# Performance work log

Hardware: AMD Instinct MI355X
Metric: run time of the kernel (lower is better)

## Reference

```python
import jax, jax.numpy as jnp
import numpy as np
import math

B, S, D, H, L, V, MAXLEN = 4, 2047, 256, 8, 2, 32000, 2048
DK = D // H
DFF = 2 * D
EPS = 1e-5


def make_pe(max_len, d):
    pos = jnp.arange(max_len, dtype=jnp.float32)[:, None]
    div = jnp.exp(jnp.arange(0, d, 2, dtype=jnp.float32) * (-math.log(10000.0) / d))
    pe = jnp.zeros((max_len, d), dtype=jnp.float32)
    pe = pe.at[:, 0::2].set(jnp.sin(pos * div))
    pe = pe.at[:, 1::2].set(jnp.cos(pos * div))
    return pe[None]  # [1, max_len, d]


def setup_inputs() -> dict:
    key = jax.random.key(0)
    ks = jax.random.split(key, 16)
    s = 0.02
    T = S + 1
    return {
        "embeddings": jax.random.normal(ks[0], (B, D), jnp.float32),
        "output_tokens": jax.random.randint(ks[1], (B, S), 0, V, jnp.int64),
        "causal_mask": jnp.tril(jnp.ones((T, T), jnp.int32))[None, None],  # [1,1,T,T]
        "key_padding_mask": jnp.ones((B, 1, 1, T), jnp.int32),
        "tok_emb": jax.random.normal(ks[2], (V, D), jnp.float32) * s,
        "pe": make_pe(MAXLEN, D),
        "Wq": jax.random.normal(ks[3], (L, D, D), jnp.float32) * s,
        "Wk": jax.random.normal(ks[4], (L, D, D), jnp.float32) * s,
        "Wv": jax.random.normal(ks[5], (L, D, D), jnp.float32) * s,
        "Wo": jax.random.normal(ks[6], (L, D, D), jnp.float32) * s,
        "bo": jnp.zeros((L, D), jnp.float32),
        "ln1_g": jnp.ones((L, D), jnp.float32),
        "ln1_b": jnp.zeros((L, D), jnp.float32),
        "W1": jax.random.normal(ks[7], (L, D, DFF), jnp.float32) * s,
        "b1": jnp.zeros((L, DFF), jnp.float32),
        "W2": jax.random.normal(ks[8], (L, DFF, D), jnp.float32) * s,
        "b2": jnp.zeros((L, D), jnp.float32),
        "ln2_g": jnp.ones((L, D), jnp.float32),
        "ln2_b": jnp.zeros((L, D), jnp.float32),
    }


def layer_norm(x, g, b):
    mu = jnp.mean(x, axis=-1, keepdims=True)
    var = jnp.mean(jnp.square(x - mu), axis=-1, keepdims=True)
    return (x - mu) * jax.lax.rsqrt(var + EPS) * g + b


def attention(x, Wq, Wk, Wv, Wo, bo, causal_mask, key_padding_mask):
    b, t, d = x.shape
    q = (x @ Wq).reshape(b, t, H, DK)
    k = (x @ Wk).reshape(b, t, H, DK)
    v = (x @ Wv).reshape(b, t, H, DK)
    scores = jnp.einsum('bqhd,bkhd->bhqk', q, k) / math.sqrt(DK)  # [B,H,T,T]
    neg = jnp.float32(-jnp.inf)
    scores = jnp.where(causal_mask == 0, neg, scores)
    scores = jnp.where(key_padding_mask == 0, neg, scores)
    attn = jax.nn.softmax(scores, axis=-1)
    out = jnp.einsum('bhqk,bkhd->bqhd', attn, v).reshape(b, t, d)
    return out @ Wo + bo


def reference(embeddings, output_tokens, causal_mask, key_padding_mask,
              tok_emb, pe, Wq, Wk, Wv, Wo, bo, ln1_g, ln1_b,
              W1, b1, W2, b2, ln2_g, ln2_b):
    emb_tok = tok_emb[output_tokens]                       # [B,S,D]
    x = jnp.concatenate([embeddings[:, None, :], emb_tok], axis=1)  # [B,T,D]
    x = x + pe[:, :x.shape[1]]
    for l in range(L):
        a = attention(x, Wq[l], Wk[l], Wv[l], Wo[l], bo[l], causal_mask, key_padding_mask)
        x = layer_norm(x + a, ln1_g[l], ln1_b[l])
        ff = jax.nn.relu(x @ W1[l] + b1[l]) @ W2[l] + b2[l]
        x = layer_norm(x + ff, ln2_g[l], ln2_b[l])
    return x[:, 1:, :]  # drop the prepended embedding position
```

## Files before the change

kernel.cpp:

```cpp
#include <hip/hip_runtime.h>
#include <cstdint>
#include <cstddef>

#define B_   4
#define S_   2047
#define T_   2048
#define D_   256
#define H_   8
#define DK_  32
#define DFF_ 512
#define L_   2

typedef short          s8v  __attribute__((ext_vector_type(8)));
typedef float          f4v  __attribute__((ext_vector_type(4)));
typedef unsigned short u4v  __attribute__((ext_vector_type(4)));
typedef unsigned short u8v  __attribute__((ext_vector_type(8)));
typedef unsigned int   u2v  __attribute__((ext_vector_type(2)));
typedef unsigned int   uint32;

union U8 { u8v v; unsigned short e[8]; };

__device__ __forceinline__ float bf2f(unsigned short h) {
    unsigned int u = ((unsigned int)h) << 16;
    float f; __builtin_memcpy(&f, &u, 4); return f;
}
__device__ __forceinline__ unsigned short f2bf(float f) {
    unsigned int u; __builtin_memcpy(&u, &f, 4);
    u += 0x7fffu + ((u >> 16) & 1u);
    return (unsigned short)(u >> 16);
}
__device__ __forceinline__ uint32 pack_bf2(float lo, float hi) {
    uint32 a, b;
    __builtin_memcpy(&a, &lo, 4); __builtin_memcpy(&b, &hi, 4);
    a += 0x8000u; b += 0x8000u;
    return __builtin_amdgcn_perm(b, a, 0x07060302);
}

#define QSCALE2 0.25503485951542068f

__global__ __launch_bounds__(256) void prep_k(
    const float* __restrict__ emb, const int* __restrict__ toks,
    const float* __restrict__ tokE, const float* __restrict__ pe,
    unsigned short* __restrict__ X,
    const float* __restrict__ Wq, const float* __restrict__ Wk,
    const float* __restrict__ Wv, const float* __restrict__ Wo,
    const float* __restrict__ W1, const float* __restrict__ W2,
    unsigned short* __restrict__ WqkvT, unsigned short* __restrict__ WoT,
    unsigned short* __restrict__ W1T, unsigned short* __restrict__ W2T)
{
    __shared__ float tile[32][33];
    if (blockIdx.x < 1024) {
        int idx = blockIdx.x * 256 + threadIdx.x;
        int d8 = (idx & 31) * 8;
        int t  = (idx >> 5) & (T_ - 1);
        int b  = idx >> 16;
        const float* src = (t == 0) ? (emb + b * D_)
                                    : (tokE + (size_t)toks[b * S_ + t - 1] * D_);
        const float* p = pe + (size_t)t * D_ + d8;
        U8 o;
#pragma unroll
        for (int j = 0; j < 8; ++j) o.e[j] = f2bf(src[d8 + j] + p[j]);
        *(u8v*)(X + (size_t)(b * T_ + t) * D_ + d8) = o.v;
        return;
    }
    int idx = blockIdx.x - 1024;
    const float* src; unsigned short* dst; int R, C, tr, tc;
    if (idx < 512) {
        int w = idx >> 7, rem = idx & 127, l = rem >> 6, t = rem & 63;
        tr = t >> 3; tc = t & 7; R = 256; C = 256;
        src = (w == 0 ? Wq : w == 1 ? Wk : w == 2 ? Wv : Wo) + (size_t)l * 65536;
        dst = (w < 3) ? WqkvT + (size_t)l * 196608 + (size_t)w * 65536
                      : WoT + (size_t)l * 65536;
    } else if (idx < 768) {
        int rem = idx - 512, l = rem >> 7, t = rem & 127;
        tr = t >> 4; tc = t & 15; R = 256; C = 512;
        src = W1 + (size_t)l * 131072; dst = W1T + (size_t)l * 131072;
    } else {
        int rem = idx - 768, l = rem >> 7, t = rem & 127;
        tr = t >> 3; tc = t & 7; R = 512; C = 256;
        src = W2 + (size_t)l * 131072; dst = W2T + (size_t)l * 131072;
    }
    int x = threadIdx.x & 31, y = threadIdx.x >> 5;
    int r0 = tr * 32, c0 = tc * 32;
#pragma unroll
    for (int i = 0; i < 32; i += 8) tile[y + i][x] = src[(size_t)(r0 + y + i) * C + c0 + x];
    __syncthreads();
#pragma unroll
    for (int i = 0; i < 32; i += 8)
        dst[(size_t)(c0 + y + i) * R + r0 + x] = f2bf(tile[x][y + i]);
}

__global__ __launch_bounds__(256) void gemm64_k(
    const unsigned short* __restrict__ A, const unsigned short* __restrict__ WT,
    const float* __restrict__ bias,
    unsigned short* __restrict__ oq, unsigned short* __restrict__ ok,
    unsigned short* __restrict__ ov, unsigned short* __restrict__ out,
    int K, int Ntot, int mode)
{
    __shared__ unsigned short At[64 * 72];
    __shared__ unsigned short Wt[64 * 72];
    const int tid = threadIdx.x;
    const int wave = tid >> 6, lane = tid & 63, l15 = lane & 15, quad = lane >> 4;
    const int m0 = blockIdx.x * 64, n0g = blockIdx.y * 64;

    f4v acc[4];
#pragma unroll
    for (int i = 0; i < 4; ++i) acc[i] = (f4v){0.f, 0.f, 0.f, 0.f};

    const int arow = tid >> 2, acg = (tid & 3) * 16;
    const unsigned short* ag = A + (size_t)(m0 + arow) * K + acg;
    const unsigned short* wg = WT + (size_t)(n0g + arow) * K + acg;
    u8v a0 = *(const u8v*)ag, a1 = *(const u8v*)(ag + 8);
    u8v w0 = *(const u8v*)wg, w1 = *(const u8v*)(wg + 8);

    const int niter = K >> 6;
    for (int kk = 0; kk < niter; ++kk) {
        *(u8v*)&At[arow * 72 + acg] = a0; *(u8v*)&At[arow * 72 + acg + 8] = a1;
        *(u8v*)&Wt[arow * 72 + acg] = w0; *(u8v*)&Wt[arow * 72 + acg + 8] = w1;
        __syncthreads();
        if (kk + 1 < niter) {
            int o = (kk + 1) * 64;
            a0 = *(const u8v*)(ag + o); a1 = *(const u8v*)(ag + o + 8);
            w0 = *(const u8v*)(wg + o); w1 = *(const u8v*)(wg + o + 8);
        }
#pragma unroll
        for (int ks = 0; ks < 2; ++ks) {
            s8v aF = *(const s8v*)&At[(wave * 16 + l15) * 72 + ks * 32 + quad * 8];
#pragma unroll
            for (int nt = 0; nt < 4; ++nt) {
                s8v wF = *(const s8v*)&Wt[(nt * 16 + l15) * 72 + ks * 32 + quad * 8];
                acc[nt] = __builtin_amdgcn_mfma_f32_16x16x32_bf16(aF, wF, acc[nt], 0, 0, 0);
            }
        }
        __syncthreads();
    }

    const int b = m0 >> 11, t0 = m0 & (T_ - 1);
    if (mode == 0) {
        int sub = blockIdx.y >> 2;
        int cb  = (blockIdx.y & 3) * 64;
        if (sub < 2) {
            unsigned short* dst = sub ? ok : oq;
            float sc = sub ? 1.f : QSCALE2;
#pragma unroll
            for (int nt = 0; nt < 4; ++nt) {
                int c = cb + nt * 16 + l15, hh = c >> 5, dk = c & 31;
#pragma unroll
                for (int r = 0; r < 4; ++r) {
                    int t = t0 + wave * 16 + quad * 4 + r;
                    dst[((size_t)(b * H_ + hh) * T_ + t) * DK_ + dk] = f2bf(acc[nt][r] * sc);
                }
            }
        } else {
            unsigned short* Vb = At;
#pragma unroll
            for (int nt = 0; nt < 4; ++nt) {
                int base = (nt * 16 + l15) * 72 + wave * 16 + quad * 4;
                *(uint32*)&Vb[base]     = pack_bf2(acc[nt][0], acc[nt][1]);
                *(uint32*)&Vb[base + 2] = pack_bf2(acc[nt][2], acc[nt][3]);
            }
            __syncthreads();
            int c = tid >> 2, chunk = tid & 3;
            int cg = cb + c, hh = cg >> 5, dk = cg & 31;
            unsigned short* dst = ov + ((size_t)(b * H_ + hh) * DK_ + dk) * T_ + t0 + chunk * 16;
            u8v v0 = *(u8v*)&Vb[c * 72 + chunk * 16];
            u8v v1 = *(u8v*)&Vb[c * 72 + chunk * 16 + 8];
            *(u8v*)dst = v0; *(u8v*)(dst + 8) = v1;
        }
    } else {
#pragma unroll
        for (int nt = 0; nt < 4; ++nt) {
            int c = n0g + nt * 16 + l15;
            float bv = bias[c];
#pragma unroll
            for (int r = 0; r < 4; ++r) {
                float v = acc[nt][r] + bv;
                v = v > 0.f ? v : 0.f;
                out[(size_t)(m0 + wave * 16 + quad * 4 + r) * Ntot + c] = f2bf(v);
            }
        }
    }
}

__global__ __launch_bounds__(256) void gemm16_k(
    const unsigned short* __restrict__ A, const unsigned short* __restrict__ WT,
    const float* __restrict__ bias, const unsigned short* __restrict__ resid,
    const float* __restrict__ gamma, const float* __restrict__ beta,
    unsigned short* __restrict__ out, int K)
{
    __shared__ unsigned short At[16 * 72];
    __shared__ unsigned short Wt[256 * 72];
    const int tid = threadIdx.x;
    const int wave = tid >> 6, lane = tid & 63, l15 = lane & 15, quad = lane >> 4;
    const int m0 = blockIdx.x * 16;

    f4v acc[4];
#pragma unroll
    for (int i = 0; i < 4; ++i) acc[i] = (f4v){0.f, 0.f, 0.f, 0.f};

    const int arow = tid >> 4, ac4 = (tid & 15) * 4;
    const unsigned short* ag = A + (size_t)(m0 + arow) * K + ac4;
    const unsigned short* wg = WT + (size_t)tid * K;
    u4v aR = *(const u4v*)ag;
    u8v wR[8];
#pragma unroll
    for (int j = 0; j < 8; ++j) wR[j] = *(const u8v*)(wg + j * 8);

    const int niter = K >> 6;
    for (int kk = 0; kk < niter; ++kk) {
        *(u4v*)&At[arow * 72 + ac4] = aR;
#pragma unroll
        for (int j = 0; j < 8; ++j) *(u8v*)&Wt[tid * 72 + j * 8] = wR[j];
        __syncthreads();
        if (kk + 1 < niter) {
            int o = (kk + 1) * 64;
            aR = *(const u4v*)(ag + o);
#pragma unroll
            for (int j = 0; j < 8; ++j) wR[j] = *(const u8v*)(wg + o + j * 8);
        }
#pragma unroll
        for (int ks = 0; ks < 2; ++ks) {
            s8v aF = *(const s8v*)&At[l15 * 72 + ks * 32 + quad * 8];
#pragma unroll
            for (int nt = 0; nt < 4; ++nt) {
                s8v wF = *(const s8v*)&Wt[(wave * 64 + nt * 16 + l15) * 72 + ks * 32 + quad * 8];
                acc[nt] = __builtin_amdgcn_mfma_f32_16x16x32_bf16(aF, wF, acc[nt], 0, 0, 0);
            }
        }
        __syncthreads();
    }

    const int rbase = quad * 4;
    float* LNs = (float*)Wt;
    float* LNq = LNs + 64;
    float ps[4] = {0, 0, 0, 0}, pq[4] = {0, 0, 0, 0};
#pragma unroll
    for (int nt = 0; nt < 4; ++nt) {
        int c = wave * 64 + nt * 16 + l15;
        float bv = bias[c];
#pragma unroll
        for (int r = 0; r < 4; ++r) {
            float v = acc[nt][r] + bv + bf2f(resid[(size_t)(m0 + rbase + r) * D_ + c]);
            acc[nt][r] = v;
            ps[r] += v; pq[r] += v * v;
        }
    }
#pragma unroll
    for (int r = 0; r < 4; ++r) {
        float s = ps[r], q = pq[r];
        s += __shfl_xor(s, 1); q += __shfl_xor(q, 1);
        s += __shfl_xor(s, 2); q += __shfl_xor(q, 2);
        s += __shfl_xor(s, 4); q += __shfl_xor(q, 4);
        s += __shfl_xor(s, 8); q += __shfl_xor(q, 8);
        if (l15 == 0) { LNs[(rbase + r) * 4 + wave] = s; LNq[(rbase + r) * 4 + wave] = q; }
    }
    __syncthreads();
    float mu[4], rsig[4];
#pragma unroll
    for (int r = 0; r < 4; ++r) {
        int row = rbase + r;
        float s = LNs[row * 4] + LNs[row * 4 + 1] + LNs[row * 4 + 2] + LNs[row * 4 + 3];
        float q = LNq[row * 4] + LNq[row * 4 + 1] + LNq[row * 4 + 2] + LNq[row * 4 + 3];
        float m = s * (1.f / 256.f);
        mu[r] = m;
        rsig[r] = rsqrtf(q * (1.f / 256.f) - m * m + 1e-5f);
    }
#pragma unroll
    for (int nt = 0; nt < 4; ++nt) {
        int c = wave * 64 + nt * 16 + l15;
        float g = gamma[c], be = beta[c];
#pragma unroll
        for (int r = 0; r < 4; ++r)
            out[(size_t)(m0 + rbase + r) * D_ + c] =
                f2bf((acc[nt][r] - mu[r]) * rsig[r] * g + be);
    }
}

__global__ __launch_bounds__(256) void attn_k(
    const unsigned short* __restrict__ Qh, const unsigned short* __restrict__ Kh,
    const unsigned short* __restrict__ VT, unsigned short* __restrict__ AO)
{
    __shared__ unsigned short Kt[128 * 40];
    __shared__ unsigned short Vt[32 * 144];
    __shared__ unsigned short Ps[4][16 * 136];

    const int tid = threadIdx.x, wave = tid >> 6, lane = tid & 63;
    const int l15 = lane & 15, quad = lane >> 4;
    const int bh = blockIdx.y, b = bh >> 3, h = bh & 7;
    const size_t hoff = (size_t)bh * T_ * DK_;
    unsigned short* Pw = &Ps[wave][0];

    const int qts[2] = { (int)blockIdx.x, 31 - (int)blockIdx.x };
    const int nk0 = qts[0] / 2 + 1, nk1 = qts[1] / 2 + 1;
    const int ntot = nk0 + nk1;

    const int krow = tid >> 1, khalf = (tid & 1) * 16;
    const int vdk = tid >> 3, vc = (tid & 7) * 16;
    const unsigned short* kgp = Kh + hoff + (size_t)krow * DK_ + khalf;
    const unsigned short* vgp = VT + ((size_t)bh * DK_ + vdk) * T_ + vc;

    u8v kr0 = *(const u8v*)kgp, kr1 = *(const u8v*)(kgp + 8);
    u8v vr0 = *(const u8v*)vgp, vr1 = *(const u8v*)(vgp + 8);

    s8v qB = {0,0,0,0,0,0,0,0};
    f4v O0 = {0,0,0,0}, O1 = {0,0,0,0};
    float l_i = 0.f;
    int nkt = 0, q0w = 0;

    for (int it = 0; it < ntot; ++it) {
        const int phase = (it >= nk0);
        const int kt = phase ? it - nk0 : it;
        if (kt == 0) {
            int qt = qts[phase]; nkt = phase ? nk1 : nk0;
            q0w = qt * 64 + wave * 16;
            qB = *(const s8v*)(Qh + hoff + (size_t)(q0w + l15) * DK_ + quad * 8);
            O0 = (f4v){0,0,0,0}; O1 = (f4v){0,0,0,0};
            l_i = 0.f;
        }
        *(u8v*)&Kt[krow * 40 + khalf]     = kr0;
        *(u8v*)&Kt[krow * 40 + khalf + 8] = kr1;
        *(u8v*)&Vt[vdk * 144 + vc]        = vr0;
        *(u8v*)&Vt[vdk * 144 + vc + 8]    = vr1;
        __syncthreads();
        {
            int itn = it + 1;
            if (itn < ntot) {
                int ktn = (itn >= nk0) ? itn - nk0 : itn;
                const unsigned short* kn = kgp + (size_t)ktn * 128 * DK_;
                const unsigned short* vn = vgp + (size_t)ktn * 128;
                kr0 = *(const u8v*)kn; kr1 = *(const u8v*)(kn + 8);
                vr0 = *(const u8v*)vn; vr1 = *(const u8v*)(vn + 8);
            }
        }
        const int k0 = kt * 128;

        f4v s[8];
        f4v zero = {0,0,0,0};
#pragma unroll
        for (int nt = 0; nt < 8; ++nt) {
            s8v kA = *(const s8v*)&Kt[(nt * 16 + l15) * 40 + quad * 8];
            s[nt] = __builtin_amdgcn_mfma_f32_16x16x32_bf16(kA, qB, zero, 0, 0, 0);
        }
        if (kt == nkt - 1) {
            int query = q0w + l15;
#pragma unroll
            for (int nt = 0; nt < 8; ++nt)
#pragma unroll
                for (int r = 0; r < 4; ++r) {
                    int key = k0 + nt * 16 + quad * 4 + r;
                    if (key > query) s[nt][r] = -1e30f;
                }
        }
        float rs = 0.f;
#pragma unroll
        for (int nt = 0; nt < 8; ++nt)
#pragma unroll
            for (int r = 0; r < 4; ++r) {
                float p = exp2f(s[nt][r]);
                s[nt][r] = p;
                rs += p;
            }
        rs += __shfl_xor(rs, 16);
        rs += __shfl_xor(rs, 32);
        l_i += rs;
#pragma unroll
        for (int nt = 0; nt < 8; ++nt) {
            u2v pw;
            pw.x = pack_bf2(s[nt][0], s[nt][1]);
            pw.y = pack_bf2(s[nt][2], s[nt][3]);
            *(u2v*)&Pw[l15 * 136 + nt * 16 + quad * 4] = pw;
        }
#pragma unroll
        for (int ks = 0; ks < 4; ++ks) {
            s8v aP = *(const s8v*)&Pw[l15 * 136 + ks * 32 + quad * 8];
            s8v v0 = *(const s8v*)&Vt[l15 * 144 + ks * 32 + quad * 8];
            s8v v1 = *(const s8v*)&Vt[(16 + l15) * 144 + ks * 32 + quad * 8];
            O0 = __builtin_amdgcn_mfma_f32_16x16x32_bf16(aP, v0, O0, 0, 0, 0);
            O1 = __builtin_amdgcn_mfma_f32_16x16x32_bf16(aP, v1, O1, 0, 0, 0);
        }
        if (kt == nkt - 1) {
#pragma unroll
            for (int r = 0; r < 4; ++r) {
                float linv = 1.f / __shfl(l_i, quad * 4 + r);
                int row = q0w + quad * 4 + r;
                size_t base = (size_t)(b * T_ + row) * D_ + h * DK_;
                AO[base + l15]      = f2bf(O0[r] * linv);
                AO[base + 16 + l15] = f2bf(O1[r] * linv);
            }
        }
        __syncthreads();
    }
}

__global__ __launch_bounds__(256) void copyout_k(
    const unsigned short* __restrict__ X, float* __restrict__ out)
{
    int idx = blockIdx.x * 256 + threadIdx.x;
    if (idx >= B_ * S_ * (D_ / 8)) return;
    int d8 = (idx & 31) * 8;
    int s  = (idx >> 5) % S_;
    int b  = (idx >> 5) / S_;
    U8 v; v.v = *(const u8v*)(X + ((size_t)(b * T_ + s + 1)) * D_ + d8);
    float* o = out + ((size_t)b * S_ + s) * D_ + d8;
#pragma unroll
    for (int j = 0; j < 8; ++j) o[j] = bf2f(v.e[j]);
}

extern "C" void kernel_launch(void* const* d_in, const int* in_sizes, int n_in,
                              void* d_out, int out_size, void* d_ws, size_t ws_size,
                              hipStream_t stream)
{
    const float* emb  = (const float*)d_in[0];
    const int*   toks = (const int*)d_in[1];
    const float* tokE = (const float*)d_in[4];
    const float* pe   = (const float*)d_in[5];
    const float* Wq   = (const float*)d_in[6];
    const float* Wk   = (const float*)d_in[7];
    const float* Wv   = (const float*)d_in[8];
    const float* Wo   = (const float*)d_in[9];
    const float* bo   = (const float*)d_in[10];
    const float* g1   = (const float*)d_in[11];
    const float* be1  = (const float*)d_in[12];
    const float* W1   = (const float*)d_in[13];
    const float* b1   = (const float*)d_in[14];
    const float* W2   = (const float*)d_in[15];
    const float* b2   = (const float*)d_in[16];
    const float* g2   = (const float*)d_in[17];
    const float* be2  = (const float*)d_in[18];
    float* out = (float*)d_out;

    unsigned short* ws = (unsigned short*)d_ws;
    size_t off = 0;
    const size_t XSZ = (size_t)B_ * T_ * D_;
    unsigned short* Xa    = ws + off; off += XSZ;
    unsigned short* Xb    = ws + off; off += XSZ;
    unsigned short* Qh    = ws + off; off += XSZ;
    unsigned short* Kh    = ws + off; off += XSZ;
    unsigned short* VTb   = ws + off; off += XSZ;
    unsigned short* AOb   = ws + off; off += XSZ;
    unsigned short* Hb    = ws + off; off += (size_t)B_ * T_ * DFF_;
    unsigned short* WqkvT = ws + off; off += (size_t)L_ * 3 * D_ * D_;
    unsigned short* WoT   = ws + off; off += (size_t)L_ * D_ * D_;
    unsigned short* W1T   = ws + off; off += (size_t)L_ * D_ * DFF_;
    unsigned short* W2T   = ws + off; off += (size_t)L_ * DFF_ * D_;
    (void)ws_size; (void)in_sizes; (void)n_in; (void)out_size;

    prep_k<<<dim3(2048), 256, 0, stream>>>(emb, toks, tokE, pe, Xa,
                                           Wq, Wk, Wv, Wo, W1, W2,
                                           WqkvT, WoT, W1T, W2T);

    for (int l = 0; l < L_; ++l) {
        const unsigned short* wqkv = WqkvT + (size_t)l * 3 * D_ * D_;
        const unsigned short* wo   = WoT + (size_t)l * D_ * D_;
        const unsigned short* w1   = W1T + (size_t)l * D_ * DFF_;
        const unsigned short* w2   = W2T + (size_t)l * DFF_ * D_;

        gemm64_k<<<dim3(128, 12), 256, 0, stream>>>(Xa, wqkv, nullptr,
                                                    Qh, Kh, VTb, nullptr, D_, D_, 0);
        attn_k<<<dim3(16, 32), 256, 0, stream>>>(Qh, Kh, VTb, AOb);
        gemm16_k<<<dim3(512), 256, 0, stream>>>(AOb, wo, bo + l * D_, Xa,
                                                g1 + l * D_, be1 + l * D_, Xb, D_);
        gemm64_k<<<dim3(128, 8), 256, 0, stream>>>(Xb, w1, b1 + l * DFF_,
                                                   nullptr, nullptr, nullptr, Hb, D_, DFF_, 1);
        gemm16_k<<<dim3(512), 256, 0, stream>>>(Hb, w2, b2 + l * D_, Xb,
                                                g2 + l * D_, be2 + l * D_, Xa, DFF_);
    }
    copyout_k<<<dim3(1024), 256, 0, stream>>>(Xa, out);
}
```

Baseline: 285.1 us.

## Fuse Wo projection, LN1, FFN and LN2 into one per-row-tile kernel

```diff
diff --git a/kernel.cpp b/kernel.cpp
--- a/kernel.cpp
+++ b/kernel.cpp
@@ -182,100 +182,6 @@
     }
 }
 
-__global__ __launch_bounds__(256) void gemm16_k(
-    const unsigned short* __restrict__ A, const unsigned short* __restrict__ WT,
-    const float* __restrict__ bias, const unsigned short* __restrict__ resid,
-    const float* __restrict__ gamma, const float* __restrict__ beta,
-    unsigned short* __restrict__ out, int K)
-{
-    __shared__ unsigned short At[16 * 72];
-    __shared__ unsigned short Wt[256 * 72];
-    const int tid = threadIdx.x;
-    const int wave = tid >> 6, lane = tid & 63, l15 = lane & 15, quad = lane >> 4;
-    const int m0 = blockIdx.x * 16;
-
-    f4v acc[4];
-#pragma unroll
-    for (int i = 0; i < 4; ++i) acc[i] = (f4v){0.f, 0.f, 0.f, 0.f};
-
-    const int arow = tid >> 4, ac4 = (tid & 15) * 4;
-    const unsigned short* ag = A + (size_t)(m0 + arow) * K + ac4;
-    const unsigned short* wg = WT + (size_t)tid * K;
-    u4v aR = *(const u4v*)ag;
-    u8v wR[8];
-#pragma unroll
-    for (int j = 0; j < 8; ++j) wR[j] = *(const u8v*)(wg + j * 8);
-
-    const int niter = K >> 6;
-    for (int kk = 0; kk < niter; ++kk) {
-        *(u4v*)&At[arow * 72 + ac4] = aR;
-#pragma unroll
-        for (int j = 0; j < 8; ++j) *(u8v*)&Wt[tid * 72 + j * 8] = wR[j];
-        __syncthreads();
-        if (kk + 1 < niter) {
-            int o = (kk + 1) * 64;
-            aR = *(const u4v*)(ag + o);
-#pragma unroll
-            for (int j = 0; j < 8; ++j) wR[j] = *(const u8v*)(wg + o + j * 8);
-        }
-#pragma unroll
-        for (int ks = 0; ks < 2; ++ks) {
-            s8v aF = *(const s8v*)&At[l15 * 72 + ks * 32 + quad * 8];
-#pragma unroll
-            for (int nt = 0; nt < 4; ++nt) {
-                s8v wF = *(const s8v*)&Wt[(wave * 64 + nt * 16 + l15) * 72 + ks * 32 + quad * 8];
-                acc[nt] = __builtin_amdgcn_mfma_f32_16x16x32_bf16(aF, wF, acc[nt], 0, 0, 0);
-            }
-        }
-        __syncthreads();
-    }
-
-    const int rbase = quad * 4;
-    float* LNs = (float*)Wt;
-    float* LNq = LNs + 64;
-    float ps[4] = {0, 0, 0, 0}, pq[4] = {0, 0, 0, 0};
-#pragma unroll
-    for (int nt = 0; nt < 4; ++nt) {
-        int c = wave * 64 + nt * 16 + l15;
-        float bv = bias[c];
-#pragma unroll
-        for (int r = 0; r < 4; ++r) {
-            float v = acc[nt][r] + bv + bf2f(resid[(size_t)(m0 + rbase + r) * D_ + c]);
-            acc[nt][r] = v;
-            ps[r] += v; pq[r] += v * v;
-        }
-    }
-#pragma unroll
-    for (int r = 0; r < 4; ++r) {
-        float s = ps[r], q = pq[r];
-        s += __shfl_xor(s, 1); q += __shfl_xor(q, 1);
-        s += __shfl_xor(s, 2); q += __shfl_xor(q, 2);
-        s += __shfl_xor(s, 4); q += __shfl_xor(q, 4);
-        s += __shfl_xor(s, 8); q += __shfl_xor(q, 8);
-        if (l15 == 0) { LNs[(rbase + r) * 4 + wave] = s; LNq[(rbase + r) * 4 + wave] = q; }
-    }
-    __syncthreads();
-    float mu[4], rsig[4];
-#pragma unroll
-    for (int r = 0; r < 4; ++r) {
-        int row = rbase + r;
-        float s = LNs[row * 4] + LNs[row * 4 + 1] + LNs[row * 4 + 2] + LNs[row * 4 + 3];
-        float q = LNq[row * 4] + LNq[row * 4 + 1] + LNq[row * 4 + 2] + LNq[row * 4 + 3];
-        float m = s * (1.f / 256.f);
-        mu[r] = m;
-        rsig[r] = rsqrtf(q * (1.f / 256.f) - m * m + 1e-5f);
-    }
-#pragma unroll
-    for (int nt = 0; nt < 4; ++nt) {
-        int c = wave * 64 + nt * 16 + l15;
-        float g = gamma[c], be = beta[c];
-#pragma unroll
-        for (int r = 0; r < 4; ++r)
-            out[(size_t)(m0 + rbase + r) * D_ + c] =
-                f2bf((acc[nt][r] - mu[r]) * rsig[r] * g + be);
-    }
-}
-
 __global__ __launch_bounds__(256) void attn_k(
     const unsigned short* __restrict__ Qh, const unsigned short* __restrict__ Kh,
     const unsigned short* __restrict__ VT, unsigned short* __restrict__ AO)
@@ -392,18 +298,226 @@
     }
 }
 
-__global__ __launch_bounds__(256) void copyout_k(
-    const unsigned short* __restrict__ X, float* __restrict__ out)
+template<int K>
+__device__ __forceinline__ void ldw8(s8v* dst, const unsigned short* bp, int koff) {
+#pragma unroll
+    for (int nt = 0; nt < 4; ++nt)
+#pragma unroll
+        for (int ks = 0; ks < 2; ++ks)
+            dst[nt * 2 + ks] = *(const s8v*)(bp + (size_t)nt * 16 * K + koff + ks * 32);
+}
+
+__global__ __launch_bounds__(256) void tail_k(
+    const unsigned short* __restrict__ AO,
+    const unsigned short* __restrict__ WoTl, const float* __restrict__ bo,
+    unsigned short* __restrict__ X,
+    const float* __restrict__ g1, const float* __restrict__ be1,
+    const unsigned short* __restrict__ W1Tl, const float* __restrict__ b1,
+    const unsigned short* __restrict__ W2Tl, const float* __restrict__ b2,
+    const float* __restrict__ g2, const float* __restrict__ be2,
+    float* __restrict__ fout, int last)
 {
-    int idx = blockIdx.x * 256 + threadIdx.x;
-    if (idx >= B_ * S_ * (D_ / 8)) return;
-    int d8 = (idx & 31) * 8;
-    int s  = (idx >> 5) % S_;
-    int b  = (idx >> 5) / S_;
-    U8 v; v.v = *(const u8v*)(X + ((size_t)(b * T_ + s + 1)) * D_ + d8);
-    float* o = out + ((size_t)b * S_ + s) * D_ + d8;
-#pragma unroll
-    for (int j = 0; j < 8; ++j) o[j] = bf2f(v.e[j]);
+    __shared__ unsigned short X1s[16 * 264];
+    __shared__ unsigned short Hs[16 * 520];
+    __shared__ float LNsc[128];
+
+    const int tid = threadIdx.x;
+    const int wave = tid >> 6, lane = tid & 63, l15 = lane & 15, quad = lane >> 4;
+    const int m0 = blockIdx.x * 16;
+    const int rbase = quad * 4;
+
+    const unsigned short* w0p = WoTl + (size_t)(wave * 64 + l15) * 256 + quad * 8;
+    const unsigned short* w1p = W1Tl + (size_t)(wave * 64 + l15) * 256 + quad * 8;
+    const unsigned short* w1q = W1Tl + (size_t)(256 + wave * 64 + l15) * 256 + quad * 8;
+    const unsigned short* w2p = W2Tl + (size_t)(wave * 64 + l15) * 512 + quad * 8;
+    const unsigned short* a0p = AO + (size_t)(m0 + l15) * 256 + quad * 8;
+
+    f4v acc[4];
+    s8v wb[2][8];
+    s8v ab[2][2];
+
+#pragma unroll
+    for (int i = 0; i < 4; ++i) acc[i] = (f4v){0.f, 0.f, 0.f, 0.f};
+    ldw8<256>(&wb[0][0], w0p, 0);
+    ab[0][0] = *(const s8v*)(a0p);
+    ab[0][1] = *(const s8v*)(a0p + 32);
+#pragma unroll
+    for (int kk = 0; kk < 4; ++kk) {
+        const int cur = kk & 1, nxt = cur ^ 1;
+        if (kk < 3) {
+            ldw8<256>(&wb[nxt][0], w0p, (kk + 1) * 64);
+            ab[nxt][0] = *(const s8v*)(a0p + (kk + 1) * 64);
+            ab[nxt][1] = *(const s8v*)(a0p + (kk + 1) * 64 + 32);
+        } else {
+            ldw8<256>(&wb[nxt][0], w1p, 0);
+        }
+#pragma unroll
+        for (int ks = 0; ks < 2; ++ks) {
+            s8v aF = ab[cur][ks];
+#pragma unroll
+            for (int nt = 0; nt < 4; ++nt)
+                acc[nt] = __builtin_amdgcn_mfma_f32_16x16x32_bf16(aF, wb[cur][nt * 2 + ks], acc[nt], 0, 0, 0);
+        }
+    }
+    {
+        float ps[4] = {0,0,0,0}, pq[4] = {0,0,0,0};
+#pragma unroll
+        for (int nt = 0; nt < 4; ++nt) {
+            int c = wave * 64 + nt * 16 + l15;
+            float bv = bo[c];
+#pragma unroll
+            for (int r = 0; r < 4; ++r) {
+                float v = acc[nt][r] + bv + bf2f(X[(size_t)(m0 + rbase + r) * D_ + c]);
+                acc[nt][r] = v; ps[r] += v; pq[r] += v * v;
+            }
+        }
+#pragma unroll
+        for (int r = 0; r < 4; ++r) {
+            float s = ps[r], q = pq[r];
+            s += __shfl_xor(s, 1); q += __shfl_xor(q, 1);
+            s += __shfl_xor(s, 2); q += __shfl_xor(q, 2);
+            s += __shfl_xor(s, 4); q += __shfl_xor(q, 4);
+            s += __shfl_xor(s, 8); q += __shfl_xor(q, 8);
+            if (l15 == 0) { LNsc[(rbase + r) * 4 + wave] = s; LNsc[64 + (rbase + r) * 4 + wave] = q; }
+        }
+        __syncthreads();
+        float mu[4], rsig[4];
+#pragma unroll
+        for (int r = 0; r < 4; ++r) {
+            int row = rbase + r;
+            float s = LNsc[row * 4] + LNsc[row * 4 + 1] + LNsc[row * 4 + 2] + LNsc[row * 4 + 3];
+            float q = LNsc[64 + row * 4] + LNsc[64 + row * 4 + 1] + LNsc[64 + row * 4 + 2] + LNsc[64 + row * 4 + 3];
+            float m = s * (1.f / 256.f);
+            mu[r] = m;
+            rsig[r] = rsqrtf(q * (1.f / 256.f) - m * m + 1e-5f);
+        }
+#pragma unroll
+        for (int nt = 0; nt < 4; ++nt) {
+            int c = wave * 64 + nt * 16 + l15;
+            float g = g1[c], be = be1[c];
+#pragma unroll
+            for (int r = 0; r < 4; ++r)
+                X1s[(rbase + r) * 264 + c] = f2bf((acc[nt][r] - mu[r]) * rsig[r] * g + be);
+        }
+        __syncthreads();
+    }
+
+#pragma unroll
+    for (int i = 0; i < 4; ++i) acc[i] = (f4v){0.f, 0.f, 0.f, 0.f};
+#pragma unroll
+    for (int kk = 0; kk < 4; ++kk) {
+        const int cur = kk & 1, nxt = cur ^ 1;
+        if (kk < 3) ldw8<256>(&wb[nxt][0], w1p, (kk + 1) * 64);
+        else        ldw8<256>(&wb[nxt][0], w1q, 0);
+#pragma unroll
+        for (int ks = 0; ks < 2; ++ks) {
+            s8v aF = *(const s8v*)&X1s[l15 * 264 + kk * 64 + ks * 32 + quad * 8];
+#pragma unroll
+            for (int nt = 0; nt < 4; ++nt)
+                acc[nt] = __builtin_amdgcn_mfma_f32_16x16x32_bf16(aF, wb[cur][nt * 2 + ks], acc[nt], 0, 0, 0);
+        }
+    }
+#pragma unroll
+    for (int nt = 0; nt < 4; ++nt) {
+        int c = wave * 64 + nt * 16 + l15;
+        float bv = b1[c];
+#pragma unroll
+        for (int r = 0; r < 4; ++r) {
+            float v = acc[nt][r] + bv; v = v > 0.f ? v : 0.f;
+            Hs[(rbase + r) * 520 + c] = f2bf(v);
+        }
+    }
+
+#pragma unroll
+    for (int i = 0; i < 4; ++i) acc[i] = (f4v){0.f, 0.f, 0.f, 0.f};
+#pragma unroll
+    for (int kk = 0; kk < 4; ++kk) {
+        const int cur = kk & 1, nxt = cur ^ 1;
+        if (kk < 3) ldw8<256>(&wb[nxt][0], w1q, (kk + 1) * 64);
+        else        ldw8<512>(&wb[nxt][0], w2p, 0);
+#pragma unroll
+        for (int ks = 0; ks < 2; ++ks) {
+            s8v aF = *(const s8v*)&X1s[l15 * 264 + kk * 64 + ks * 32 + quad * 8];
+#pragma unroll
+            for (int nt = 0; nt < 4; ++nt)
+                acc[nt] = __builtin_amdgcn_mfma_f32_16x16x32_bf16(aF, wb[cur][nt * 2 + ks], acc[nt], 0, 0, 0);
+        }
+    }
+#pragma unroll
+    for (int nt = 0; nt < 4; ++nt) {
+        int c = wave * 64 + nt * 16 + l15;
+        float bv = b1[256 + c];
+#pragma unroll
+        for (int r = 0; r < 4; ++r) {
+            float v = acc[nt][r] + bv; v = v > 0.f ? v : 0.f;
+            Hs[(rbase + r) * 520 + 256 + c] = f2bf(v);
+        }
+    }
+    __syncthreads();
+
+#pragma unroll
+    for (int i = 0; i < 4; ++i) acc[i] = (f4v){0.f, 0.f, 0.f, 0.f};
+#pragma unroll
+    for (int kk = 0; kk < 8; ++kk) {
+        const int cur = kk & 1, nxt = cur ^ 1;
+        if (kk < 7) ldw8<512>(&wb[nxt][0], w2p, (kk + 1) * 64);
+#pragma unroll
+        for (int ks = 0; ks < 2; ++ks) {
+            s8v aF = *(const s8v*)&Hs[l15 * 520 + kk * 64 + ks * 32 + quad * 8];
+#pragma unroll
+            for (int nt = 0; nt < 4; ++nt)
+                acc[nt] = __builtin_amdgcn_mfma_f32_16x16x32_bf16(aF, wb[cur][nt * 2 + ks], acc[nt], 0, 0, 0);
+        }
+    }
+    {
+        float ps[4] = {0,0,0,0}, pq[4] = {0,0,0,0};
+#pragma unroll
+        for (int nt = 0; nt < 4; ++nt) {
+            int c = wave * 64 + nt * 16 + l15;
+            float bv = b2[c];
+#pragma unroll
+            for (int r = 0; r < 4; ++r) {
+                float v = acc[nt][r] + bv + bf2f(X1s[(rbase + r) * 264 + c]);
+                acc[nt][r] = v; ps[r] += v; pq[r] += v * v;
+            }
+        }
+#pragma unroll
+        for (int r = 0; r < 4; ++r) {
+            float s = ps[r], q = pq[r];
+            s += __shfl_xor(s, 1); q += __shfl_xor(q, 1);
+            s += __shfl_xor(s, 2); q += __shfl_xor(q, 2);
+            s += __shfl_xor(s, 4); q += __shfl_xor(q, 4);
+            s += __shfl_xor(s, 8); q += __shfl_xor(q, 8);
+            if (l15 == 0) { LNsc[(rbase + r) * 4 + wave] = s; LNsc[64 + (rbase + r) * 4 + wave] = q; }
+        }
+        __syncthreads();
+        float mu[4], rsig[4];
+#pragma unroll
+        for (int r = 0; r < 4; ++r) {
+            int row = rbase + r;
+            float s = LNsc[row * 4] + LNsc[row * 4 + 1] + LNsc[row * 4 + 2] + LNsc[row * 4 + 3];
+            float q = LNsc[64 + row * 4] + LNsc[64 + row * 4 + 1] + LNsc[64 + row * 4 + 2] + LNsc[64 + row * 4 + 3];
+            float m = s * (1.f / 256.f);
+            mu[r] = m;
+            rsig[r] = rsqrtf(q * (1.f / 256.f) - m * m + 1e-5f);
+        }
+#pragma unroll
+        for (int nt = 0; nt < 4; ++nt) {
+            int c = wave * 64 + nt * 16 + l15;
+            float g = g2[c], be = be2[c];
+#pragma unroll
+            for (int r = 0; r < 4; ++r) {
+                float val = (acc[nt][r] - mu[r]) * rsig[r] * g + be;
+                if (!last) {
+                    X[(size_t)(m0 + rbase + r) * D_ + c] = f2bf(val);
+                } else {
+                    int gr = m0 + rbase + r;
+                    int t = gr & (T_ - 1), bb = gr >> 11;
+                    if (t) fout[((size_t)bb * S_ + t - 1) * D_ + c] = val;
+                }
+            }
+        }
+    }
 }
 
 extern "C" void kernel_launch(void* const* d_in, const int* in_sizes, int n_in,
@@ -444,6 +558,7 @@
     unsigned short* W1T   = ws + off; off += (size_t)L_ * D_ * DFF_;
     unsigned short* W2T   = ws + off; off += (size_t)L_ * DFF_ * D_;
     (void)ws_size; (void)in_sizes; (void)n_in; (void)out_size;
+    (void)Xb; (void)Hb;
 
     prep_k<<<dim3(2048), 256, 0, stream>>>(emb, toks, tokE, pe, Xa,
                                            Wq, Wk, Wv, Wo, W1, W2,
@@ -458,12 +573,11 @@
         gemm64_k<<<dim3(128, 12), 256, 0, stream>>>(Xa, wqkv, nullptr,
                                                     Qh, Kh, VTb, nullptr, D_, D_, 0);
         attn_k<<<dim3(16, 32), 256, 0, stream>>>(Qh, Kh, VTb, AOb);
-        gemm16_k<<<dim3(512), 256, 0, stream>>>(AOb, wo, bo + l * D_, Xa,
-                                                g1 + l * D_, be1 + l * D_, Xb, D_);
-        gemm64_k<<<dim3(128, 8), 256, 0, stream>>>(Xb, w1, b1 + l * DFF_,
-                                                   nullptr, nullptr, nullptr, Hb, D_, DFF_, 1);
-        gemm16_k<<<dim3(512), 256, 0, stream>>>(Hb, w2, b2 + l * D_, Xb,
-                                                g2 + l * D_, be2 + l * D_, Xa, DFF_);
-    }
-    copyout_k<<<dim3(1024), 256, 0, stream>>>(Xa, out);
-}
+        tail_k<<<dim3(512), 256, 0, stream>>>(AOb, wo, bo + l * D_, Xa,
+                                              g1 + l * D_, be1 + l * D_,
+                                              w1, b1 + l * DFF_,
+                                              w2, b2 + l * D_,
+                                              g2 + l * D_, be2 + l * D_,
+                                              out, l == L_ - 1);
+    }
+}
```

Measured after the change: 291.8 us. 1.02x slower.

## Use 32-row LN GEMM tiles and fuse final output copy into last GEMM

Applied to the files above, without the earlier changes.

```diff
diff --git a/kernel.cpp b/kernel.cpp
--- a/kernel.cpp
+++ b/kernel.cpp
@@ -182,61 +182,66 @@
     }
 }
 
-__global__ __launch_bounds__(256) void gemm16_k(
+__global__ __launch_bounds__(512) void gemm32ln_k(
     const unsigned short* __restrict__ A, const unsigned short* __restrict__ WT,
     const float* __restrict__ bias, const unsigned short* __restrict__ resid,
     const float* __restrict__ gamma, const float* __restrict__ beta,
-    unsigned short* __restrict__ out, int K)
+    unsigned short* __restrict__ Xout, float* __restrict__ fout,
+    int K, int last)
 {
-    __shared__ unsigned short At[16 * 72];
+    __shared__ unsigned short At[32 * 72];
     __shared__ unsigned short Wt[256 * 72];
+    __shared__ float LNsc[256];
+
     const int tid = threadIdx.x;
     const int wave = tid >> 6, lane = tid & 63, l15 = lane & 15, quad = lane >> 4;
-    const int m0 = blockIdx.x * 16;
+    const int wr = wave >> 2, wc = wave & 3;
+    const int m0 = blockIdx.x * 32;
 
     f4v acc[4];
 #pragma unroll
     for (int i = 0; i < 4; ++i) acc[i] = (f4v){0.f, 0.f, 0.f, 0.f};
 
-    const int arow = tid >> 4, ac4 = (tid & 15) * 4;
-    const unsigned short* ag = A + (size_t)(m0 + arow) * K + ac4;
-    const unsigned short* wg = WT + (size_t)tid * K;
-    u4v aR = *(const u4v*)ag;
-    u8v wR[8];
-#pragma unroll
-    for (int j = 0; j < 8; ++j) wR[j] = *(const u8v*)(wg + j * 8);
+    const int arow = tid >> 3, acol = (tid & 7) * 8;
+    const int wrow = tid >> 1, wcol = (tid & 1) * 32;
+    const unsigned short* ag = A + (size_t)(m0 + (arow & 31)) * K + acol;
+    const unsigned short* wg = WT + (size_t)wrow * K + wcol;
+    u8v a0 = {0,0,0,0,0,0,0,0};
+    if (tid < 256) a0 = *(const u8v*)ag;
+    u8v w0 = *(const u8v*)wg,        w1 = *(const u8v*)(wg + 8);
+    u8v w2 = *(const u8v*)(wg + 16), w3 = *(const u8v*)(wg + 24);
 
     const int niter = K >> 6;
     for (int kk = 0; kk < niter; ++kk) {
-        *(u4v*)&At[arow * 72 + ac4] = aR;
-#pragma unroll
-        for (int j = 0; j < 8; ++j) *(u8v*)&Wt[tid * 72 + j * 8] = wR[j];
+        if (tid < 256) *(u8v*)&At[arow * 72 + acol] = a0;
+        *(u8v*)&Wt[wrow * 72 + wcol]      = w0;
+        *(u8v*)&Wt[wrow * 72 + wcol + 8]  = w1;
+        *(u8v*)&Wt[wrow * 72 + wcol + 16] = w2;
+        *(u8v*)&Wt[wrow * 72 + wcol + 24] = w3;
         __syncthreads();
         if (kk + 1 < niter) {
             int o = (kk + 1) * 64;
-            aR = *(const u4v*)(ag + o);
-#pragma unroll
-            for (int j = 0; j < 8; ++j) wR[j] = *(const u8v*)(wg + o + j * 8);
+            if (tid < 256) a0 = *(const u8v*)(ag + o);
+            w0 = *(const u8v*)(wg + o);      w1 = *(const u8v*)(wg + o + 8);
+            w2 = *(const u8v*)(wg + o + 16); w3 = *(const u8v*)(wg + o + 24);
         }
 #pragma unroll
         for (int ks = 0; ks < 2; ++ks) {
-            s8v aF = *(const s8v*)&At[l15 * 72 + ks * 32 + quad * 8];
+            s8v aF = *(const s8v*)&At[(wr * 16 + l15) * 72 + ks * 32 + quad * 8];
 #pragma unroll
             for (int nt = 0; nt < 4; ++nt) {
-                s8v wF = *(const s8v*)&Wt[(wave * 64 + nt * 16 + l15) * 72 + ks * 32 + quad * 8];
+                s8v wF = *(const s8v*)&Wt[(wc * 64 + nt * 16 + l15) * 72 + ks * 32 + quad * 8];
                 acc[nt] = __builtin_amdgcn_mfma_f32_16x16x32_bf16(aF, wF, acc[nt], 0, 0, 0);
             }
         }
         __syncthreads();
     }
 
-    const int rbase = quad * 4;
-    float* LNs = (float*)Wt;
-    float* LNq = LNs + 64;
+    const int rbase = wr * 16 + quad * 4;
     float ps[4] = {0, 0, 0, 0}, pq[4] = {0, 0, 0, 0};
 #pragma unroll
     for (int nt = 0; nt < 4; ++nt) {
-        int c = wave * 64 + nt * 16 + l15;
+        int c = wc * 64 + nt * 16 + l15;
         float bv = bias[c];
 #pragma unroll
         for (int r = 0; r < 4; ++r) {
@@ -252,27 +257,37 @@
         s += __shfl_xor(s, 2); q += __shfl_xor(q, 2);
         s += __shfl_xor(s, 4); q += __shfl_xor(q, 4);
         s += __shfl_xor(s, 8); q += __shfl_xor(q, 8);
-        if (l15 == 0) { LNs[(rbase + r) * 4 + wave] = s; LNq[(rbase + r) * 4 + wave] = q; }
+        if (l15 == 0) {
+            LNsc[(rbase + r) * 4 + wc]       = s;
+            LNsc[128 + (rbase + r) * 4 + wc] = q;
+        }
     }
     __syncthreads();
     float mu[4], rsig[4];
 #pragma unroll
     for (int r = 0; r < 4; ++r) {
         int row = rbase + r;
-        float s = LNs[row * 4] + LNs[row * 4 + 1] + LNs[row * 4 + 2] + LNs[row * 4 + 3];
-        float q = LNq[row * 4] + LNq[row * 4 + 1] + LNq[row * 4 + 2] + LNq[row * 4 + 3];
+        float s = LNsc[row * 4] + LNsc[row * 4 + 1] + LNsc[row * 4 + 2] + LNsc[row * 4 + 3];
+        float q = LNsc[128 + row * 4] + LNsc[128 + row * 4 + 1] + LNsc[128 + row * 4 + 2] + LNsc[128 + row * 4 + 3];
         float m = s * (1.f / 256.f);
         mu[r] = m;
         rsig[r] = rsqrtf(q * (1.f / 256.f) - m * m + 1e-5f);
     }
 #pragma unroll
     for (int nt = 0; nt < 4; ++nt) {
-        int c = wave * 64 + nt * 16 + l15;
+        int c = wc * 64 + nt * 16 + l15;
         float g = gamma[c], be = beta[c];
 #pragma unroll
-        for (int r = 0; r < 4; ++r)
-            out[(size_t)(m0 + rbase + r) * D_ + c] =
-                f2bf((acc[nt][r] - mu[r]) * rsig[r] * g + be);
+        for (int r = 0; r < 4; ++r) {
+            float val = (acc[nt][r] - mu[r]) * rsig[r] * g + be;
+            if (!last) {
+                Xout[(size_t)(m0 + rbase + r) * D_ + c] = f2bf(val);
+            } else {
+                int gr = m0 + rbase + r;
+                int t = gr & (T_ - 1), bb = gr >> 11;
+                if (t) fout[((size_t)bb * S_ + t - 1) * D_ + c] = val;
+            }
+        }
     }
 }
 
@@ -390,20 +405,6 @@
         }
         __syncthreads();
     }
-}
-
-__global__ __launch_bounds__(256) void copyout_k(
-    const unsigned short* __restrict__ X, float* __restrict__ out)
-{
-    int idx = blockIdx.x * 256 + threadIdx.x;
-    if (idx >= B_ * S_ * (D_ / 8)) return;
-    int d8 = (idx & 31) * 8;
-    int s  = (idx >> 5) % S_;
-    int b  = (idx >> 5) / S_;
-    U8 v; v.v = *(const u8v*)(X + ((size_t)(b * T_ + s + 1)) * D_ + d8);
-    float* o = out + ((size_t)b * S_ + s) * D_ + d8;
-#pragma unroll
-    for (int j = 0; j < 8; ++j) o[j] = bf2f(v.e[j]);
 }
 
 extern "C" void kernel_launch(void* const* d_in, const int* in_sizes, int n_in,
@@ -454,16 +455,18 @@
         const unsigned short* wo   = WoT + (size_t)l * D_ * D_;
         const unsigned short* w1   = W1T + (size_t)l * D_ * DFF_;
         const unsigned short* w2   = W2T + (size_t)l * DFF_ * D_;
+        const int last = (l == L_ - 1);
 
         gemm64_k<<<dim3(128, 12), 256, 0, stream>>>(Xa, wqkv, nullptr,
                                                     Qh, Kh, VTb, nullptr, D_, D_, 0);
         attn_k<<<dim3(16, 32), 256, 0, stream>>>(Qh, Kh, VTb, AOb);
-        gemm16_k<<<dim3(512), 256, 0, stream>>>(AOb, wo, bo + l * D_, Xa,
-                                                g1 + l * D_, be1 + l * D_, Xb, D_);
+        gemm32ln_k<<<dim3(256), 512, 0, stream>>>(AOb, wo, bo + l * D_, Xa,
+                                                  g1 + l * D_, be1 + l * D_,
+                                                  Xb, nullptr, D_, 0);
         gemm64_k<<<dim3(128, 8), 256, 0, stream>>>(Xb, w1, b1 + l * DFF_,
                                                    nullptr, nullptr, nullptr, Hb, D_, DFF_, 1);
-        gemm16_k<<<dim3(512), 256, 0, stream>>>(Hb, w2, b2 + l * D_, Xb,
-                                                g2 + l * D_, be2 + l * D_, Xa, DFF_);
-    }
-    copyout_k<<<dim3(1024), 256, 0, stream>>>(Xa, out);
-}
+        gemm32ln_k<<<dim3(256), 512, 0, stream>>>(Hb, w2, b2 + l * D_, Xb,
+                                                  g2 + l * D_, be2 + l * D_,
+                                                  Xa, out, DFF_, last);
+    }
+}
```

New measurement: 261.5 us. 8.3% less time.
